# Kernel optimization log

Hardware: AMD Instinct MI355X
Metric: run time of the kernel (lower is better)

The kernel has to match this reference:

```python
import jax, jax.numpy as jnp
import numpy as np

IN_FEATURES = 4096
OUT_FEATURES = 11008
TOKENS = 32


def ternarize_weight(w):
    # abs-mean scale, clamped; threshold at 0.7*abs_mean
    abs_mean = jnp.maximum(jnp.mean(jnp.abs(w)), 1e-5)
    threshold = 0.7 * abs_mean
    q = jnp.where(w > threshold, 1.0, jnp.where(w < -threshold, -1.0, 0.0))
    # straight-through estimator: forward value q*abs_mean, grad passes to w
    return w + jax.lax.stop_gradient(q * abs_mean - w)


def setup_inputs() -> dict:
    key = jax.random.key(0)
    kx, kw = jax.random.split(key)
    x = jax.random.normal(kx, (TOKENS, IN_FEATURES), dtype=jnp.float32)
    # master fp32 weights, init std = 1/sqrt(in_features) as in the module
    weight = jax.random.normal(kw, (OUT_FEATURES, IN_FEATURES), dtype=jnp.float32) / np.sqrt(IN_FEATURES)
    return {"x": x, "weight": weight}


def reference(x, weight):
    # ternary_active=True, ternary_alpha=1.0 path: fully ternarized weights
    w_q = ternarize_weight(weight)
    # F.linear(x, w): [T, in] @ [out, in]^T -> [T, out]
    return jnp.einsum('ti,oi->to', x, w_q)
```

## Files before the change

### kernel.cpp

```cpp
#include <hip/hip_runtime.h>
#include <hip/hip_bf16.h>
#include <stdint.h>

#define IN_F 4096
#define OUT_F 11008
#define TOKENS 32
#define NELEM_W (OUT_F * IN_F)
#define OUT_ELEMS (TOKENS * OUT_F)

typedef __attribute__((ext_vector_type(8))) __bf16 bf16x8;
typedef __attribute__((ext_vector_type(4))) float  f32x4;

#define XB_OFF    64
#define GPART_OFF 262208
#define APART_OFF 3080256

__device__ __forceinline__ uint32_t bfr(float v) {
    uint32_t u = __float_as_uint(v);
    uint32_t r = u + 0x7FFFu + ((u >> 16) & 1u);
    return r >> 16;
}

#define ABSUM_BLOCKS 2048
#define XCVT_BLOCKS  64

__global__ __launch_bounds__(256) void absum_xcvt_kernel(const float* __restrict__ w,
                                                         const float* __restrict__ x,
                                                         float* __restrict__ apart,
                                                         uint4* __restrict__ xb) {
    if (blockIdx.x >= ABSUM_BLOCKS) {
        int i = (blockIdx.x - ABSUM_BLOCKS) * 256 + threadIdx.x;
        const float4* x4 = (const float4*)x;
        float4 a0 = x4[i * 2];
        float4 a1 = x4[i * 2 + 1];
        uint4 o;
        o.x = bfr(a0.x) | (bfr(a0.y) << 16);
        o.y = bfr(a0.z) | (bfr(a0.w) << 16);
        o.z = bfr(a1.x) | (bfr(a1.y) << 16);
        o.w = bfr(a1.z) | (bfr(a1.w) << 16);
        xb[i] = o;
        return;
    }
    int tid = blockIdx.x * blockDim.x + threadIdx.x;
    int stride = ABSUM_BLOCKS * 256;
    const float4* w4 = (const float4*)w;
    const int n4 = NELEM_W / 4;
    float s = 0.f;
    for (int i = tid; i < n4; i += stride) {
        float4 v = w4[i];
        s += fabsf(v.x) + fabsf(v.y) + fabsf(v.z) + fabsf(v.w);
    }
    for (int off = 32; off > 0; off >>= 1)
        s += __shfl_down(s, off, 64);
    __shared__ float wsum[4];
    int lane = threadIdx.x & 63;
    int wv   = threadIdx.x >> 6;
    if (lane == 0) wsum[wv] = s;
    __syncthreads();
    if (threadIdx.x == 0)
        apart[blockIdx.x] = wsum[0] + wsum[1] + wsum[2] + wsum[3];
}

__global__ __launch_bounds__(256) void finalize_kernel(const float* __restrict__ apart,
                                                       float* __restrict__ wsf) {
    float s = 0.f;
#pragma unroll
    for (int j = 0; j < 8; ++j)
        s += apart[threadIdx.x + 256 * j];
    for (int off = 32; off > 0; off >>= 1)
        s += __shfl_down(s, off, 64);
    __shared__ float wsum[4];
    int lane = threadIdx.x & 63;
    int wv   = threadIdx.x >> 6;
    if (lane == 0) wsum[wv] = s;
    __syncthreads();
    if (threadIdx.x == 0) {
        double mean = (double)(wsum[0] + wsum[1] + wsum[2] + wsum[3]) / (double)NELEM_W;
        if (mean < 1e-5) mean = 1e-5;
        float mf = (float)mean;
        wsf[2] = 0.7f * mf;
        wsf[3] = mf;
    }
}

__device__ __forceinline__ uint32_t tern1(float v, float thr) {
    uint32_t u  = __float_as_uint(v);
    uint32_t pm = (u & 0x80000000u) | 0x3F800000u;
    return (__builtin_fabsf(v) > thr) ? pm : 0u;
}

__device__ __forceinline__ uint2 tern4(float4 b, float thr) {
    uint32_t q0 = tern1(b.x, thr), q1 = tern1(b.y, thr);
    uint32_t q2 = tern1(b.z, thr), q3 = tern1(b.w, thr);
    uint2 r;
    r.x = __builtin_amdgcn_perm(q1, q0, 0x07060302u);
    r.y = __builtin_amdgcn_perm(q3, q2, 0x07060302u);
    return r;
}

#define CHUNKS 16
#define WAVE_LDS 2304
#define SMEM_BYTES 4608

__global__ __launch_bounds__(128, 4) void ternary_gemm(const float* __restrict__ w,
                                                       const float* __restrict__ wsf,
                                                       const __bf16* __restrict__ xb,
                                                       float* __restrict__ gpart) {
    __shared__ char smem_raw[SMEM_BYTES];
    const float thr = wsf[2];
    const int og   = blockIdx.x >> 1;
    const int kh   = blockIdx.x & 1;
    const int tid  = threadIdx.x;
    const int wv   = tid >> 6;
    const int lane = tid & 63;
    const int col  = lane & 15;
    const int quad = lane >> 4;
    const int rlan = lane & 15;

    const int kw = kh * 2048 + wv * 1024;

    const float* wp = w + (size_t)(og * 16 + quad) * IN_F + kw + rlan * 4;
    char* stage = smem_raw + wv * WAVE_LDS;
    char* wr    = stage + quad * 144 + rlan * 8;
    const char* rd = stage + col * 144;
    const __bf16* xq = xb + (size_t)col * IN_F + kw + quad * 8;

    f32x4 acc0 = {0.f, 0.f, 0.f, 0.f};
    f32x4 acc1 = {0.f, 0.f, 0.f, 0.f};

    float4 wb[2][4];
    bf16x8 xv[2][4];

#pragma unroll
    for (int c = 0; c < 2; ++c) {
        const float*  np = wp + c * 64;
        const __bf16* xn = xq + c * 64;
        wb[c][0] = *(const float4*)(np);
        wb[c][1] = *(const float4*)(np + 4 * IN_F);
        wb[c][2] = *(const float4*)(np + 8 * IN_F);
        wb[c][3] = *(const float4*)(np + 12 * IN_F);
        xv[c][0] = *(const bf16x8*)(xn);
        xv[c][1] = *(const bf16x8*)(xn + 32);
        xv[c][2] = *(const bf16x8*)(xn + 16 * IN_F);
        xv[c][3] = *(const bf16x8*)(xn + 16 * IN_F + 32);
    }

#define GEMM_BODY(c, cur)                                                      \
    {                                                                          \
        uint2 t0 = tern4(wb[cur][0], thr);                                     \
        uint2 t1 = tern4(wb[cur][1], thr);                                     \
        uint2 t2 = tern4(wb[cur][2], thr);                                     \
        uint2 t3 = tern4(wb[cur][3], thr);                                     \
        *(uint2*)(wr)        = t0;                                             \
        *(uint2*)(wr + 576)  = t1;                                             \
        *(uint2*)(wr + 1152) = t2;                                             \
        *(uint2*)(wr + 1728) = t3;                                             \
        bf16x8 a00 = xv[cur][0], a01 = xv[cur][1];                             \
        bf16x8 a10 = xv[cur][2], a11 = xv[cur][3];                             \
        if ((c) + 2 < CHUNKS) {                                                \
            const float*  np = wp + ((c) + 2) * 64;                            \
            const __bf16* xn = xq + ((c) + 2) * 64;                            \
            wb[cur][0] = *(const float4*)(np);                                 \
            wb[cur][1] = *(const float4*)(np + 4 * IN_F);                      \
            wb[cur][2] = *(const float4*)(np + 8 * IN_F);                      \
            wb[cur][3] = *(const float4*)(np + 12 * IN_F);                     \
            xv[cur][0] = *(const bf16x8*)(xn);                                 \
            xv[cur][1] = *(const bf16x8*)(xn + 32);                            \
            xv[cur][2] = *(const bf16x8*)(xn + 16 * IN_F);                     \
            xv[cur][3] = *(const bf16x8*)(xn + 16 * IN_F + 32);                \
        }                                                                      \
        bf16x8 bw0 = *(const bf16x8*)(rd + quad * 16);                         \
        bf16x8 bw1 = *(const bf16x8*)(rd + 64 + quad * 16);                    \
        acc0 = __builtin_amdgcn_mfma_f32_16x16x32_bf16(a00, bw0, acc0, 0, 0, 0); \
        acc1 = __builtin_amdgcn_mfma_f32_16x16x32_bf16(a10, bw0, acc1, 0, 0, 0); \
        acc0 = __builtin_amdgcn_mfma_f32_16x16x32_bf16(a01, bw1, acc0, 0, 0, 0); \
        acc1 = __builtin_amdgcn_mfma_f32_16x16x32_bf16(a11, bw1, acc1, 0, 0, 0); \
    }

    for (int c = 0; c < CHUNKS; c += 2) {
        GEMM_BODY(c, 0)
        GEMM_BODY(c + 1, 1)
    }
#undef GEMM_BODY

    __syncthreads();
    float* red  = (float*)smem_raw;
    float* base = red + wv * 512;
#pragma unroll
    for (int r = 0; r < 4; ++r) base[r * 64 + lane]       = acc0[r];
#pragma unroll
    for (int r = 0; r < 4; ++r) base[256 + r * 64 + lane] = acc1[r];
    __syncthreads();

    float* gp = gpart + (size_t)kh * OUT_ELEMS;
    for (int p = tid; p < 512; p += 128) {
        int t = p >> 4, cc = p & 15;
        int a = t >> 4;
        int q = (t >> 2) & 3;
        int r = t & 3;
        int idx = a * 256 + r * 64 + q * 16 + cc;
        gp[(size_t)t * OUT_F + og * 16 + cc] = red[idx] + red[512 + idx];
    }
}

__global__ __launch_bounds__(256) void combine_kernel(const float* __restrict__ gpart,
                                                      const float* __restrict__ wsf,
                                                      float* __restrict__ out) {
    const float sc = wsf[3];
    int i = blockIdx.x * 256 + threadIdx.x;
    const float4* p0 = (const float4*)gpart;
    const float4* p1 = (const float4*)(gpart + OUT_ELEMS);
    float4 a = p0[i], b = p1[i];
    float4 o;
    o.x = (a.x + b.x) * sc;
    o.y = (a.y + b.y) * sc;
    o.z = (a.z + b.z) * sc;
    o.w = (a.w + b.w) * sc;
    ((float4*)out)[i] = o;
}

extern "C" void kernel_launch(void* const* d_in, const int* in_sizes, int n_in,
                              void* d_out, int out_size, void* d_ws, size_t ws_size,
                              hipStream_t stream) {
    const float* x = (const float*)d_in[0];
    const float* w = (const float*)d_in[1];
    float* out     = (float*)d_out;
    char* ws       = (char*)d_ws;

    float* wsf     = (float*)ws;
    uint4* xb      = (uint4*)(ws + XB_OFF);
    float* gpart   = (float*)(ws + GPART_OFF);
    float* apart   = (float*)(ws + APART_OFF);

    absum_xcvt_kernel<<<ABSUM_BLOCKS + XCVT_BLOCKS, 256, 0, stream>>>(w, x, apart, xb);
    finalize_kernel<<<1, 256, 0, stream>>>(apart, wsf);
    ternary_gemm<<<(OUT_F / 16) * 2, 128, 0, stream>>>(w, wsf, (const __bf16*)(ws + XB_OFF), gpart);
    combine_kernel<<<OUT_ELEMS / 4 / 256, 256, 0, stream>>>(gpart, wsf, out);
}
```

Measured before the change: 279.4 us.

## Fold finalize and combine into GEMM, use 4-wave blocks covering full K

```diff
diff --git a/kernel.cpp b/kernel.cpp
--- a/kernel.cpp
+++ b/kernel.cpp
@@ -7,13 +7,13 @@
 #define TOKENS 32
 #define NELEM_W (OUT_F * IN_F)
 #define OUT_ELEMS (TOKENS * OUT_F)
+#define NBLK 688
 
 typedef __attribute__((ext_vector_type(8))) __bf16 bf16x8;
 typedef __attribute__((ext_vector_type(4))) float  f32x4;
 
-#define XB_OFF    64
-#define GPART_OFF 262208
-#define APART_OFF 3080256
+#define APART_OFF 0
+#define XB_OFF    4096
 
 __device__ __forceinline__ uint32_t bfr(float v) {
     uint32_t u = __float_as_uint(v);
@@ -21,15 +21,13 @@
     return r >> 16;
 }
 
-#define ABSUM_BLOCKS 2048
-#define XCVT_BLOCKS  64
-
 __global__ __launch_bounds__(256) void absum_xcvt_kernel(const float* __restrict__ w,
                                                          const float* __restrict__ x,
                                                          float* __restrict__ apart,
                                                          uint4* __restrict__ xb) {
-    if (blockIdx.x >= ABSUM_BLOCKS) {
-        int i = (blockIdx.x - ABSUM_BLOCKS) * 256 + threadIdx.x;
+    const int tid = threadIdx.x;
+    if (blockIdx.x < 64) {
+        int i = blockIdx.x * 256 + tid;
         const float4* x4 = (const float4*)x;
         float4 a0 = x4[i * 2];
         float4 a1 = x4[i * 2 + 1];
@@ -39,48 +37,23 @@
         o.z = bfr(a1.x) | (bfr(a1.y) << 16);
         o.w = bfr(a1.z) | (bfr(a1.w) << 16);
         xb[i] = o;
-        return;
-    }
-    int tid = blockIdx.x * blockDim.x + threadIdx.x;
-    int stride = ABSUM_BLOCKS * 256;
-    const float4* w4 = (const float4*)w;
-    const int n4 = NELEM_W / 4;
+    }
+    const float4* wb4 = (const float4*)(w + (size_t)blockIdx.x * (16 * IN_F));
     float s = 0.f;
-    for (int i = tid; i < n4; i += stride) {
-        float4 v = w4[i];
+#pragma unroll 4
+    for (int i = tid; i < 16384; i += 256) {
+        float4 v = wb4[i];
         s += fabsf(v.x) + fabsf(v.y) + fabsf(v.z) + fabsf(v.w);
     }
     for (int off = 32; off > 0; off >>= 1)
         s += __shfl_down(s, off, 64);
     __shared__ float wsum[4];
-    int lane = threadIdx.x & 63;
-    int wv   = threadIdx.x >> 6;
+    int lane = tid & 63;
+    int wv   = tid >> 6;
     if (lane == 0) wsum[wv] = s;
     __syncthreads();
-    if (threadIdx.x == 0)
+    if (tid == 0)
         apart[blockIdx.x] = wsum[0] + wsum[1] + wsum[2] + wsum[3];
-}
-
-__global__ __launch_bounds__(256) void finalize_kernel(const float* __restrict__ apart,
-                                                       float* __restrict__ wsf) {
-    float s = 0.f;
-#pragma unroll
-    for (int j = 0; j < 8; ++j)
-        s += apart[threadIdx.x + 256 * j];
-    for (int off = 32; off > 0; off >>= 1)
-        s += __shfl_down(s, off, 64);
-    __shared__ float wsum[4];
-    int lane = threadIdx.x & 63;
-    int wv   = threadIdx.x >> 6;
-    if (lane == 0) wsum[wv] = s;
-    __syncthreads();
-    if (threadIdx.x == 0) {
-        double mean = (double)(wsum[0] + wsum[1] + wsum[2] + wsum[3]) / (double)NELEM_W;
-        if (mean < 1e-5) mean = 1e-5;
-        float mf = (float)mean;
-        wsf[2] = 0.7f * mf;
-        wsf[3] = mf;
-    }
 }
 
 __device__ __forceinline__ uint32_t tern1(float v, float thr) {
@@ -100,16 +73,14 @@
 
 #define CHUNKS 16
 #define WAVE_LDS 2304
-#define SMEM_BYTES 4608
-
-__global__ __launch_bounds__(128, 4) void ternary_gemm(const float* __restrict__ w,
-                                                       const float* __restrict__ wsf,
+#define SMEM_BYTES 9216
+
+__global__ __launch_bounds__(256, 4) void ternary_gemm(const float* __restrict__ w,
+                                                       const float* __restrict__ apart,
                                                        const __bf16* __restrict__ xb,
-                                                       float* __restrict__ gpart) {
+                                                       float* __restrict__ out) {
     __shared__ char smem_raw[SMEM_BYTES];
-    const float thr = wsf[2];
-    const int og   = blockIdx.x >> 1;
-    const int kh   = blockIdx.x & 1;
+    const int og   = blockIdx.x;
     const int tid  = threadIdx.x;
     const int wv   = tid >> 6;
     const int lane = tid & 63;
@@ -117,8 +88,26 @@
     const int quad = lane >> 4;
     const int rlan = lane & 15;
 
-    const int kw = kh * 2048 + wv * 1024;
-
+    float s = 0.f;
+    for (int j = tid; j < NBLK; j += 256) s += apart[j];
+    for (int off = 32; off > 0; off >>= 1)
+        s += __shfl_down(s, off, 64);
+    float* sred = (float*)smem_raw;
+    if (lane == 0) sred[wv] = s;
+    __syncthreads();
+    if (tid == 0) {
+        double mean = (double)(sred[0] + sred[1] + sred[2] + sred[3]) / (double)NELEM_W;
+        if (mean < 1e-5) mean = 1e-5;
+        float mf = (float)mean;
+        sred[4] = 0.7f * mf;
+        sred[5] = mf;
+    }
+    __syncthreads();
+    const float thr   = sred[4];
+    const float scale = sred[5];
+    __syncthreads();
+
+    const int kw = wv * 1024;
     const float* wp = w + (size_t)(og * 16 + quad) * IN_F + kw + rlan * 4;
     char* stage = smem_raw + wv * WAVE_LDS;
     char* wr    = stage + quad * 144 + rlan * 8;
@@ -192,31 +181,16 @@
     for (int r = 0; r < 4; ++r) base[256 + r * 64 + lane] = acc1[r];
     __syncthreads();
 
-    float* gp = gpart + (size_t)kh * OUT_ELEMS;
-    for (int p = tid; p < 512; p += 128) {
+#pragma unroll
+    for (int p = tid; p < 512; p += 256) {
         int t = p >> 4, cc = p & 15;
         int a = t >> 4;
         int q = (t >> 2) & 3;
         int r = t & 3;
         int idx = a * 256 + r * 64 + q * 16 + cc;
-        gp[(size_t)t * OUT_F + og * 16 + cc] = red[idx] + red[512 + idx];
-    }
-}
-
-__global__ __launch_bounds__(256) void combine_kernel(const float* __restrict__ gpart,
-                                                      const float* __restrict__ wsf,
-                                                      float* __restrict__ out) {
-    const float sc = wsf[3];
-    int i = blockIdx.x * 256 + threadIdx.x;
-    const float4* p0 = (const float4*)gpart;
-    const float4* p1 = (const float4*)(gpart + OUT_ELEMS);
-    float4 a = p0[i], b = p1[i];
-    float4 o;
-    o.x = (a.x + b.x) * sc;
-    o.y = (a.y + b.y) * sc;
-    o.z = (a.z + b.z) * sc;
-    o.w = (a.w + b.w) * sc;
-    ((float4*)out)[i] = o;
+        float v = red[idx] + red[512 + idx] + red[1024 + idx] + red[1536 + idx];
+        out[(size_t)t * OUT_F + og * 16 + cc] = v * scale;
+    }
 }
 
 extern "C" void kernel_launch(void* const* d_in, const int* in_sizes, int n_in,
@@ -227,13 +201,9 @@
     float* out     = (float*)d_out;
     char* ws       = (char*)d_ws;
 
-    float* wsf     = (float*)ws;
+    float* apart   = (float*)(ws + APART_OFF);
     uint4* xb      = (uint4*)(ws + XB_OFF);
-    float* gpart   = (float*)(ws + GPART_OFF);
-    float* apart   = (float*)(ws + APART_OFF);
-
-    absum_xcvt_kernel<<<ABSUM_BLOCKS + XCVT_BLOCKS, 256, 0, stream>>>(w, x, apart, xb);
-    finalize_kernel<<<1, 256, 0, stream>>>(apart, wsf);
-    ternary_gemm<<<(OUT_F / 16) * 2, 128, 0, stream>>>(w, wsf, (const __bf16*)(ws + XB_OFF), gpart);
-    combine_kernel<<<OUT_ELEMS / 4 / 256, 256, 0, stream>>>(gpart, wsf, out);
-}
+
+    absum_xcvt_kernel<<<NBLK, 256, 0, stream>>>(w, x, apart, xb);
+    ternary_gemm<<<NBLK, 256, 0, stream>>>(w, apart, (const __bf16*)(ws + XB_OFF), out);
+}
```

New measurement: 282.6 us. About the same (+1.1%).
